# Kernel tuning notes

Measured on AMD Instinct MI355X. Metric: run time of the kernel, lower is better.

The kernel has to match this reference:

```python
import math
import jax, jax.numpy as jnp
import numpy as np

B, N, C = 4, 2048, 256
KMAX, RATIO, ITERS, H = 1024, 12.0, 3, 4
TAU, SIG_FLOOR, INIT_SIG_MIX, INIT_OFF, JIT = 1.0, 0.03, 0.1, 0.5, 1e-6
W_KL, W_ENT, W_OCC, W_COL = 0.05, 0.0, 0.5, 0.1
K_USE = min(max(1, math.ceil(N / RATIO)), KMAX)  # 171
EPS = 1e-8


def _sym(M):
    return 0.5 * (M + jnp.swapaxes(M, -1, -2))


def _l2n(x):
    return x / jnp.maximum(jnp.linalg.norm(x, axis=-1, keepdims=True), 1e-12)


def _ln(x, g, b):
    m = x.mean(-1, keepdims=True)
    v = ((x - m) ** 2).mean(-1, keepdims=True)
    return (x - m) / jnp.sqrt(v + 1e-5) * g + b


def setup_inputs():
    key = jax.random.key(0)
    ks = jax.random.split(key, 16)
    s = jax.random.normal(ks[0], (B, N, C), jnp.float32)
    mu = jax.random.normal(ks[1], (B, N, 3), jnp.float32)
    # per-point SPD covariances (Sigma must be PSD for the overlap solve)
    L = jax.random.normal(ks[2], (B, N, 3, 3), jnp.float32) * 0.3
    Sigma = L @ jnp.swapaxes(L, -1, -2) + 0.05 * jnp.eye(3, dtype=jnp.float32)
    mask = jnp.ones((B, N), jnp.float32)
    lim = 1.0 / math.sqrt(C)
    u = lambda k, sh: jax.random.uniform(k, sh, jnp.float32, -lim, lim)
    return dict(
        s=s, mu=mu, Sigma=Sigma, mask=mask,
        slot_embed_pool=jax.random.normal(ks[3], (KMAX, C), jnp.float32) * 0.02,
        geo_offsets_pool=jax.random.normal(ks[4], (KMAX, 3), jnp.float32) * 0.5,
        gating_W=u(ks[5], (C, C)), proj_q_W=u(ks[6], (C, C)), proj_k_W=u(ks[7], (C, C)),
        gru_w_ih=u(ks[8], (3 * C, C)), gru_w_hh=u(ks[9], (3 * C, C)),
        gru_b_ih=u(ks[10], (3 * C,)), gru_b_hh=u(ks[11], (3 * C,)),
        ln_g=jnp.ones((C,), jnp.float32), ln_b=jnp.zeros((C,), jnp.float32),
        mlp_w1=u(ks[12], (4 * C, C)), mlp_b1=u(ks[13], (4 * C,)),
        mlp_w2=u(ks[14], (C, 4 * C)), mlp_b2=u(ks[15], (C,)),
        w_geo=jnp.float32(1.0),
        geo_scale_raw=jnp.full((H,), -4.0, jnp.float32),
        geo_bias=jnp.full((H,), -6.0, jnp.float32),
    )


def _forward(s, mu, Sigma, mask, slot_embed_pool, geo_offsets_pool, gating_W,
             proj_q_W, proj_k_W, gru_w_ih, gru_w_hh, gru_b_ih, gru_b_hh,
             ln_g, ln_b, mlp_w1, mlp_b1, mlp_w2, mlp_b2,
             w_geo, geo_scale_raw, geo_bias):
    I3 = jnp.eye(3, dtype=s.dtype)
    m1 = mask[:, :, None]                    # [B,N,1]
    cnt = jnp.maximum(mask.sum(1), EPS)      # [B]

    # ---- slot selection (eval mode: no gate noise, rand_slots=0) ----
    s_global = (s * m1).sum(1) / cnt[:, None]
    q = _l2n(s_global @ gating_W.T)
    kn = _l2n(slot_embed_pool)
    scores = q @ kn.T                        # [B,KMAX]
    idx = jax.lax.top_k(scores, K_USE)[1]    # [B,K]
    slots = slot_embed_pool[idx]             # [B,K,C]
    geo_off = geo_offsets_pool[idx]          # [B,K,3]

    # ---- masked mean/std of mu ----
    mean = (mu * m1).sum(1) / cnt[:, None]   # [B,3]
    dm = mu - mean[:, None, :]
    cov = jnp.einsum('bni,bnj->bij', dm * m1, dm) / cnt[:, None, None]
    cov = _sym(cov)
    std = jnp.sqrt(jnp.maximum(jnp.diagonal(cov, axis1=-2, axis2=-1), EPS))
    std = jnp.maximum(std, SIG_FLOOR)
    mu_k = mean[:, None, :] + geo_off * (INIT_OFF * std[:, None, :])

    Sig_avg = _sym((Sigma * m1[..., None]).sum(1) / cnt[:, None, None])
    Sig_k = jnp.broadcast_to(Sig_avg[:, None] * INIT_SIG_MIX, (B, K_USE, 3, 3))
    Sig_k = Sig_k + (SIG_FLOOR ** 2) * I3 + JIT * I3

    k_sem = s @ proj_k_W.T                   # [B,N,C]
    a_h = jax.nn.softplus(geo_scale_raw)     # [H]
    A = None
    for _ in range(ITERS):
        q_sem = slots @ proj_q_W.T           # [B,K,C]
        logits_sem = jnp.einsum('bnc,bkc->bnk', k_sem, q_sem) / math.sqrt(C)
        delta = mu[:, :, None, :] - mu_k[:, None, :, :]       # [B,N,K,3]
        sig_sum = Sigma[:, :, None] + Sig_k[:, None]          # [B,N,K,3,3]
        sol = jnp.linalg.solve(sig_sum, delta[..., None])[..., 0]
        maha = (delta * sol).sum(-1)
        logdet = jnp.linalg.slogdet(sig_sum)[1]
        G = -0.5 * (maha + logdet)                            # [B,N,K]
        geo = (a_h[None, :, None, None] * G[:, None] + geo_bias[None, :, None, None]).sum(1)
        logits = (logits_sem + w_geo * geo) / max(TAU, 1e-6)
        logits = jnp.where(m1 < 0.5, -1e9, logits)
        A = jax.nn.softmax(logits, axis=-1) * m1              # [B,N,K]
        # moment-matching merge (A already mask-weighted; matches torch A*mask)
        occ = jnp.maximum(A.sum(1), EPS)                      # [B,K]
        mu_k = jnp.einsum('bnk,bni->bki', A, mu) / occ[..., None]
        d = mu[:, :, None, :] - mu_k[:, None, :, :]
        outer = d[..., :, None] * d[..., None, :]             # [B,N,K,3,3]
        Sig_k = (jnp.einsum('bnk,bnij->bkij', A, Sigma)
                 + jnp.einsum('bnk,bnkij->bkij', A, outer)) / occ[:, :, None, None]
        Sig_k = _sym(Sig_k) + max(JIT, 1e-6) * I3
        dg = jnp.diagonal(Sig_k, axis1=-2, axis2=-1)
        dg_f = jnp.maximum(dg, SIG_FLOOR ** 2)
        Sig_k = Sig_k - I3 * dg[..., None, :] + I3 * dg_f[..., None, :]
        Sig_k = _sym(Sig_k) + JIT * I3
        denom = jnp.maximum(A.sum(1), 1e-8)
        slot_in = jnp.einsum('bnk,bnc->bkc', A, s) / denom[..., None]
        # GRU cell
        x = slot_in.reshape(-1, C)
        h = slots.reshape(-1, C)
        gi = x @ gru_w_ih.T + gru_b_ih
        gh = h @ gru_w_hh.T + gru_b_hh
        r = jax.nn.sigmoid(gi[:, :C] + gh[:, :C])
        z = jax.nn.sigmoid(gi[:, C:2 * C] + gh[:, C:2 * C])
        n = jnp.tanh(gi[:, 2 * C:] + r * gh[:, 2 * C:])
        slots = ((1.0 - z) * n + z * h).reshape(B, K_USE, C)
        xm = _ln(slots, ln_g, ln_b)
        slots = slots + (jax.nn.gelu(xm @ mlp_w1.T + mlp_b1, approximate=False) @ mlp_w2.T + mlp_b2)

    # ---- losses ----
    hist = jnp.zeros((KMAX,), jnp.float32).at[idx.reshape(-1)].add(1.0)
    p = hist / jnp.maximum(hist.sum(), 1.0)
    pc = jnp.maximum(p, 1e-8)
    usage_kl = (pc * (jnp.log(pc) - math.log(1.0 / KMAX))).sum()
    usage_neg_ent = (pc * jnp.log(pc)).sum()
    occ2 = (A * m1).sum(1)
    occ2 = occ2 / jnp.maximum(occ2.sum(-1, keepdims=True), 1e-8)
    occ_mse = ((occ2 - 1.0 / K_USE) ** 2).mean()
    X = jnp.swapaxes(A * m1, 1, 2)           # [B,K,N]
    Xn = X / jnp.maximum(jnp.linalg.norm(X, axis=-1, keepdims=True), 1e-8)
    Gm = jnp.einsum('bkn,bln->bkl', Xn, Xn)
    eyeK = jnp.eye(K_USE, dtype=A.dtype)[None]
    off = (Gm - eyeK) * (1.0 - eyeK)
    col = (off ** 2).mean()
    total = W_KL * usage_kl + W_ENT * usage_neg_ent + W_OCC * occ_mse + W_COL * col
    return (A, slots, mu_k, Sig_k, idx, usage_kl, usage_neg_ent, occ_mse, col, total)


def reference(s, mu, Sigma, mask, slot_embed_pool, geo_offsets_pool, gating_W,
              proj_q_W, proj_k_W, gru_w_ih, gru_w_hh, gru_b_ih, gru_b_hh,
              ln_g, ln_b, mlp_w1, mlp_b1, mlp_w2, mlp_b2,
              w_geo, geo_scale_raw, geo_bias):
    return _forward(s, mu, Sigma, mask, slot_embed_pool, geo_offsets_pool, gating_W,
                    proj_q_W, proj_k_W, gru_w_ih, gru_w_hh, gru_b_ih, gru_b_hh,
                    ln_g, ln_b, mlp_w1, mlp_b1, mlp_w2, mlp_b2,
                    w_geo, geo_scale_raw, geo_bias)
```

## Files before the change

kernel.cpp:

```cpp
#include <hip/hip_runtime.h>
#include <math.h>

#define B_ 4
#define N_ 2048
#define C_ 256
#define KMAX_ 1024
#define KU_ 171
#define BK_ 684
#define ITERS_ 3
#define H_ 4
#define EPS_ 1e-8f
#define SIGF_ 0.03f
#define JIT_ 1e-6f
#define LOGKMAX_ 6.93147180559945f

#define WS_CNT 0
#define WS_MUS 4
#define WS_MOS 16
#define WS_SGS 40
#define WS_COLACC 100
#define WS_SSUM 128
#define WS_STATS_BYTES (1152*4)
#define WS_MEAN 1152
#define WS_STD 1164
#define WS_SIGAVG 1176
#define WS_IDXI 1216
#define WS_KSEM 1920
#define WS_QSEM (WS_KSEM+2097152)
#define WS_OCC  (WS_QSEM+175104)
#define WS_PART (WS_OCC+704)
#define WS_W2P  WS_PART
#define WS_GBUF (WS_PART+1400832)
#define WS_ATA  WS_GBUF
#define WS_SNEW (WS_GBUF+700416)
#define WS_HID  (WS_SNEW+175104)
#define WS_ACPART (WS_HID+700416)
#define WS_QV   (WS_ACPART+28160)
#define WS_SCORE (WS_QV+1024)

#define O_A 0
#define O_SLOTS 1400832
#define O_MUK   1575936
#define O_SIGK  1577988
#define O_IDX   1584144
#define O_KL    1584828
#define O_ENT   1584829
#define O_OCC   1584830
#define O_COL   1584831
#define O_TOT   1584832

__device__ __forceinline__ float wred(float v) {
  #pragma unroll
  for (int i = 32; i; i >>= 1) v += __shfl_xor(v, i);
  return v;
}
__device__ __forceinline__ float wmax(float v) {
  #pragma unroll
  for (int i = 32; i; i >>= 1) v = fmaxf(v, __shfl_xor(v, i));
  return v;
}

__device__ __forceinline__ float blk_red(float v, float* red, int t) {
  red[t] = v; __syncthreads();
  #pragma unroll
  for (int s = 128; s > 0; s >>= 1) {
    if (t < s) red[t] += red[t + s];
    __syncthreads();
  }
  float r = red[0]; __syncthreads();
  return r;
}

__global__ __launch_bounds__(256) void k_mom(const float* __restrict__ mu,
    const float* __restrict__ Sigma, const float* __restrict__ mask,
    float* __restrict__ ws) {
  int blk = blockIdx.x; int b = blk / 8; int nc = blk % 8; int t = threadIdx.x;
  int n = nc * 256 + t;
  float m = mask[b * N_ + n];
  const float* mun = mu + ((size_t)(b * N_ + n)) * 3;
  float m0 = mun[0], m1v = mun[1], m2 = mun[2];
  const float* sgn = Sigma + ((size_t)(b * N_ + n)) * 9;
  float sg[9];
  #pragma unroll
  for (int j = 0; j < 9; j++) sg[j] = sgn[j];
  int lane = t & 63;
  float vals[19];
  vals[0] = m; vals[1] = m * m0; vals[2] = m * m1v; vals[3] = m * m2;
  vals[4] = m * m0 * m0; vals[5] = m * m0 * m1v; vals[6] = m * m0 * m2;
  vals[7] = m * m1v * m1v; vals[8] = m * m1v * m2; vals[9] = m * m2 * m2;
  #pragma unroll
  for (int j = 0; j < 9; j++) vals[10 + j] = m * sg[j];
  #pragma unroll
  for (int j = 0; j < 19; j++) {
    float v = wred(vals[j]);
    if (lane == 0) {
      int base = (j == 0) ? WS_CNT + b : (j < 4 ? WS_MUS + b * 3 + (j - 1)
                 : (j < 10 ? WS_MOS + b * 6 + (j - 4) : WS_SGS + b * 9 + (j - 10)));
      atomicAdd(ws + base, v);
    }
  }
}

__global__ __launch_bounds__(256) void k_ssum(const float* __restrict__ s,
    const float* __restrict__ mask, float* __restrict__ ws) {
  int blk = blockIdx.x; int b = blk / 64; int nc = blk % 64; int t = threadIdx.x;
  const float* sb = s + ((size_t)b * N_ + nc * 32) * C_;
  const float* mk = mask + b * N_ + nc * 32;
  float sa = 0.f;
  #pragma unroll 8
  for (int nn = 0; nn < 32; nn++) sa += mk[nn] * sb[(size_t)nn * C_ + t];
  atomicAdd(ws + WS_SSUM + b * C_ + t, sa);
}

__global__ __launch_bounds__(256) void k_qv(float* __restrict__ ws,
    const float* __restrict__ gW, float* __restrict__ qv_o) {
  int b = blockIdx.x, t = threadIdx.x;
  __shared__ float sb[C_];
  __shared__ float rv[256];
  sb[t] = ws[WS_SSUM + b * C_ + t];
  __syncthreads();
  if (blockIdx.x == 0 && t < B_) {
    int bb = t;
    float cnt = fmaxf(ws[WS_CNT + bb], EPS_);
    float me[3];
    #pragma unroll
    for (int i = 0; i < 3; i++) { me[i] = ws[WS_MUS + bb * 3 + i] / cnt; ws[WS_MEAN + bb * 3 + i] = me[i]; }
    const int dg[3] = {0, 3, 5};
    #pragma unroll
    for (int i = 0; i < 3; i++) {
      float cov = ws[WS_MOS + bb * 6 + dg[i]] / cnt - me[i] * me[i];
      ws[WS_STD + bb * 3 + i] = fmaxf(sqrtf(fmaxf(cov, EPS_)), SIGF_);
    }
    #pragma unroll
    for (int i = 0; i < 3; i++)
      #pragma unroll
      for (int j = 0; j < 3; j++)
        ws[WS_SIGAVG + bb * 9 + i * 3 + j] =
            0.5f * (ws[WS_SGS + bb * 9 + i * 3 + j] + ws[WS_SGS + bb * 9 + j * 3 + i]) / cnt;
  }
  const float4* g4 = (const float4*)(gW + (size_t)t * C_);
  float qr = 0.f;
  #pragma unroll 4
  for (int c4 = 0; c4 < 64; c4++) {
    float4 g = g4[c4];
    qr += sb[c4 * 4] * g.x + sb[c4 * 4 + 1] * g.y + sb[c4 * 4 + 2] * g.z + sb[c4 * 4 + 3] * g.w;
  }
  float n2 = blk_red(qr * qr, rv, t);
  qv_o[b * C_ + t] = qr / fmaxf(sqrtf(n2), 1e-12f);
}

__global__ __launch_bounds__(256) void k_score(const float* __restrict__ qv,
    const float* __restrict__ pool, float* __restrict__ score) {
  int blk = blockIdx.x; int b = blk >> 4; int pc = blk & 15;
  int t = threadIdx.x; int row = pc * 64 + (t >> 2); int q = t & 3;
  __shared__ float qs[C_];
  qs[t] = qv[b * C_ + t];
  __syncthreads();
  const float4* p4 = (const float4*)(pool + (size_t)row * C_ + q * 64);
  float d = 0.f, p2 = 0.f;
  #pragma unroll
  for (int i = 0; i < 16; i++) {
    float4 pv = p4[i];
    int c = q * 64 + i * 4;
    d += qs[c] * pv.x + qs[c + 1] * pv.y + qs[c + 2] * pv.z + qs[c + 3] * pv.w;
    p2 += pv.x * pv.x + pv.y * pv.y + pv.z * pv.z + pv.w * pv.w;
  }
  d += __shfl_xor(d, 1); d += __shfl_xor(d, 2);
  p2 += __shfl_xor(p2, 1); p2 += __shfl_xor(p2, 2);
  if (q == 0) score[b * KMAX_ + row] = d / fmaxf(sqrtf(p2), 1e-12f);
}

__global__ __launch_bounds__(256) void k_sort(const float* __restrict__ score,
    int* __restrict__ idx_o, float* __restrict__ idxf_o) {
  int b = blockIdx.x, t = threadIdx.x;
  __shared__ float val[KMAX_]; __shared__ int id[KMAX_];
  for (int j = t; j < KMAX_; j += 256) { val[j] = score[b * KMAX_ + j]; id[j] = j; }
  __syncthreads();
  for (int kk = 2; kk <= KMAX_; kk <<= 1) {
    for (int j = kk >> 1; j > 0; j >>= 1) {
      for (int i = t; i < KMAX_; i += 256) {
        int ix = i ^ j;
        if (ix > i) {
          float va = val[i], vb = val[ix]; int ia = id[i], ib = id[ix];
          bool bBeforeA = (vb > va) || (vb == va && ib < ia);
          bool up = ((i & kk) == 0);
          if (up == bBeforeA) {
            val[i] = vb; val[ix] = va; id[i] = ib; id[ix] = ia;
          }
        }
      }
      __syncthreads();
    }
  }
  if (t < KU_) {
    idx_o[b * KU_ + t] = id[t];
    idxf_o[b * KU_ + t] = (float)id[t];
  }
}

__global__ __launch_bounds__(256) void k_init(const int* __restrict__ idx,
    const float* __restrict__ pool, const float* __restrict__ geop,
    const float* __restrict__ ws, float* __restrict__ slots,
    float* __restrict__ mu_k, float* __restrict__ sig_k) {
  int blk = blockIdx.x; int b = blk / KU_, k = blk % KU_; int t = threadIdx.x;
  int j = idx[b * KU_ + k];
  slots[((size_t)(b * KU_ + k)) * C_ + t] = pool[(size_t)j * C_ + t];
  if (t < 3) {
    mu_k[(b * KU_ + k) * 3 + t] = ws[WS_MEAN + b * 3 + t] + geop[j * 3 + t] * (0.5f * ws[WS_STD + b * 3 + t]);
  }
  if (t < 9) {
    float v = ws[WS_SIGAVG + b * 9 + t] * 0.1f;
    if (t == 0 || t == 4 || t == 8) v += SIGF_ * SIGF_ + JIT_;
    sig_k[((size_t)(b * KU_ + k)) * 9 + t] = v;
  }
}

__global__ __launch_bounds__(256) void k_gemm32(const float* __restrict__ in,
    const float* __restrict__ W, float* __restrict__ out, int R) {
  __shared__ float sm[32 * C_];
  int t = threadIdx.x; int r0 = blockIdx.x * 32;
  for (int i = t; i < 32 * 64; i += 256) {
    int rr = i >> 6; int r = r0 + rr;
    float4 v = {0.f, 0.f, 0.f, 0.f};
    if (r < R) v = ((const float4*)(in + (size_t)r * C_))[i & 63];
    ((float4*)sm)[i] = v;
  }
  __syncthreads();
  int cg = t & 63, rg = t >> 6;
  const float4* w0 = (const float4*)(W + (size_t)cg * C_);
  const float4* w1 = (const float4*)(W + (size_t)(cg + 64) * C_);
  const float4* w2 = (const float4*)(W + (size_t)(cg + 128) * C_);
  const float4* w3 = (const float4*)(W + (size_t)(cg + 192) * C_);
  const float4* sm4 = (const float4*)sm;
  float acc[8][4];
  #pragma unroll
  for (int a = 0; a < 8; a++)
    #pragma unroll
    for (int j = 0; j < 4; j++) acc[a][j] = 0.f;
  for (int c4 = 0; c4 < 64; c4++) {
    float4 a0 = w0[c4], a1 = w1[c4], a2 = w2[c4], a3 = w3[c4];
    #pragma unroll
    for (int a = 0; a < 8; a++) {
      float4 sv = sm4[(rg * 8 + a) * 64 + c4];
      acc[a][0] += sv.x * a0.x + sv.y * a0.y + sv.z * a0.z + sv.w * a0.w;
      acc[a][1] += sv.x * a1.x + sv.y * a1.y + sv.z * a1.z + sv.w * a1.w;
      acc[a][2] += sv.x * a2.x + sv.y * a2.y + sv.z * a2.z + sv.w * a2.w;
      acc[a][3] += sv.x * a3.x + sv.y * a3.y + sv.z * a3.z + sv.w * a3.w;
    }
  }
  #pragma unroll
  for (int a = 0; a < 8; a++) {
    int r = r0 + rg * 8 + a;
    if (r < R) {
      out[(size_t)r * C_ + cg]       = acc[a][0];
      out[(size_t)r * C_ + cg + 64]  = acc[a][1];
      out[(size_t)r * C_ + cg + 128] = acc[a][2];
      out[(size_t)r * C_ + cg + 192] = acc[a][3];
    }
  }
}

#define LG32 32
__global__ __launch_bounds__(256) void k_lgsm(const float* __restrict__ ksem,
    const float* __restrict__ qsem, const float* __restrict__ mu,
    const float* __restrict__ Sigma, const float* __restrict__ mask,
    const float* __restrict__ mu_k, const float* __restrict__ sig_k,
    const float* __restrict__ wgeo, const float* __restrict__ gsr,
    const float* __restrict__ gbias, float* __restrict__ A) {
  __shared__ float ksm[LG32 * C_];
  __shared__ float Asm[LG32][176];
  __shared__ float muk[KU_ * 3];
  __shared__ float sgk[KU_ * 6];
  __shared__ float rowd[LG32][10];
  int blk = blockIdx.x; int b = blk / (N_ / LG32); int nt = blk % (N_ / LG32);
  int t = threadIdx.x; int r0 = nt * LG32;
  for (int i = t; i < LG32 * 64; i += 256) {
    int rr = i >> 6;
    ((float4*)ksm)[i] = ((const float4*)(ksem + ((size_t)(b * N_ + r0 + rr)) * C_))[i & 63];
  }
  for (int i = t; i < KU_ * 3; i += 256) muk[i] = mu_k[(size_t)b * KU_ * 3 + i];
  for (int i = t; i < KU_ * 6; i += 256) {
    int k = i / 6, c = i % 6;
    const int map[6] = {0, 1, 2, 4, 5, 8};
    sgk[i] = sig_k[((size_t)(b * KU_ + k)) * 9 + map[c]];
  }
  for (int i = t; i < LG32 * 10; i += 256) {
    int rr = i / 10, c = i % 10;
    int n = r0 + rr;
    float v;
    if (c == 0) v = mask[b * N_ + n];
    else if (c < 4) v = mu[((size_t)(b * N_ + n)) * 3 + (c - 1)];
    else {
      const int map[6] = {0, 1, 2, 4, 5, 8};
      v = Sigma[((size_t)(b * N_ + n)) * 9 + map[c - 4]];
    }
    rowd[rr][c] = v;
  }
  __syncthreads();
  int kg = t & 63, rg = t >> 6;
  int k0i = kg, k1i = kg + 64, k2i = kg + 128;
  bool v2 = (k2i < KU_);
  const float* qbase = qsem + (size_t)b * KU_ * C_;
  const float4* q0 = (const float4*)(qbase + (size_t)k0i * C_);
  const float4* q1 = (const float4*)(qbase + (size_t)k1i * C_);
  const float4* q2 = (const float4*)(qbase + (size_t)(v2 ? k2i : k0i) * C_);
  const float4* sm4 = (const float4*)ksm;
  float acc[8][3];
  #pragma unroll
  for (int a = 0; a < 8; a++) { acc[a][0] = 0.f; acc[a][1] = 0.f; acc[a][2] = 0.f; }
  for (int c4 = 0; c4 < 64; c4++) {
    float4 qa = q0[c4], qb = q1[c4], qc = q2[c4];
    #pragma unroll
    for (int a = 0; a < 8; a++) {
      float4 sv = sm4[(rg * 8 + a) * 64 + c4];
      acc[a][0] += sv.x * qa.x + sv.y * qa.y + sv.z * qa.z + sv.w * qa.w;
      acc[a][1] += sv.x * qb.x + sv.y * qb.y + sv.z * qb.z + sv.w * qb.w;
      acc[a][2] += sv.x * qc.x + sv.y * qc.y + sv.z * qc.z + sv.w * qc.w;
    }
  }
  float ah = 0.f, bs = 0.f;
  #pragma unroll
  for (int h = 0; h < H_; h++) {
    float x = gsr[h];
    ah += fmaxf(x, 0.f) + log1pf(expf(-fabsf(x)));
    bs += gbias[h];
  }
  float wg = wgeo[0];
  #pragma unroll
  for (int kk = 0; kk < 3; kk++) {
    int k = kg + kk * 64;
    if (kk == 2 && !v2) break;
    float mk0 = muk[k * 3], mk1 = muk[k * 3 + 1], mk2 = muk[k * 3 + 2];
    float s0 = sgk[k * 6], s1 = sgk[k * 6 + 1], s2 = sgk[k * 6 + 2];
    float s3 = sgk[k * 6 + 3], s4 = sgk[k * 6 + 4], s5 = sgk[k * 6 + 5];
    #pragma unroll
    for (int a = 0; a < 8; a++) {
      int row = rg * 8 + a;
      float m = rowd[row][0];
      float d0 = rowd[row][1] - mk0, d1 = rowd[row][2] - mk1, d2 = rowd[row][3] - mk2;
      float s00 = rowd[row][4] + s0, s01 = rowd[row][5] + s1, s02 = rowd[row][6] + s2;
      float s11 = rowd[row][7] + s3, s12 = rowd[row][8] + s4, s22 = rowd[row][9] + s5;
      float c00 = s11 * s22 - s12 * s12;
      float c01 = s02 * s12 - s01 * s22;
      float c02 = s01 * s12 - s02 * s11;
      float det = s00 * c00 + s01 * c01 + s02 * c02;
      float c11 = s00 * s22 - s02 * s02;
      float c12 = s01 * s02 - s00 * s12;
      float c22 = s00 * s11 - s01 * s01;
      float inv = 1.0f / det;
      float x0 = (c00 * d0 + c01 * d1 + c02 * d2) * inv;
      float x1 = (c01 * d0 + c11 * d1 + c12 * d2) * inv;
      float x2 = (c02 * d0 + c12 * d1 + c22 * d2) * inv;
      float maha = d0 * x0 + d1 * x1 + d2 * x2;
      float logdet = logf(fmaxf(det, 1e-30f));
      float G = -0.5f * (maha + logdet);
      float l = acc[a][kk] * 0.0625f + wg * (ah * G + bs);
      if (m < 0.5f) l = -1e9f;
      Asm[row][k] = l;
    }
  }
  __syncthreads();
  int w = t >> 6, lane = t & 63;
  #pragma unroll
  for (int q = 0; q < 8; q++) {
    int a = w * 8 + q;
    float v0 = (lane < KU_) ? Asm[a][lane] : -INFINITY;
    float v1 = (lane + 64 < KU_) ? Asm[a][lane + 64] : -INFINITY;
    float vv2 = (lane + 128 < KU_) ? Asm[a][lane + 128] : -INFINITY;
    float mx = wmax(fmaxf(v0, fmaxf(v1, vv2)));
    float e0 = (lane < KU_) ? expf(v0 - mx) : 0.f;
    float e1 = (lane + 64 < KU_) ? expf(v1 - mx) : 0.f;
    float e2 = (lane + 128 < KU_) ? expf(vv2 - mx) : 0.f;
    float ss = wred(e0 + e1 + e2);
    float scale = rowd[a][0] / ss;
    if (lane < KU_) Asm[a][lane] = e0 * scale;
    if (lane + 64 < KU_) Asm[a][lane + 64] = e1 * scale;
    if (lane + 128 < KU_) Asm[a][lane + 128] = e2 * scale;
  }
  __syncthreads();
  for (int i = t; i < LG32 * KU_; i += 256) {
    int a = i / KU_, k = i - a * KU_;
    A[((size_t)(b * N_ + r0 + a)) * KU_ + k] = Asm[a][k];
  }
}

#define AC_NC 4
__global__ __launch_bounds__(256) void k_amoms(const float* __restrict__ A,
    const float* __restrict__ mu, const float* __restrict__ Sigma,
    const float* __restrict__ s, float* __restrict__ acpart,
    float* __restrict__ atpart) {
  __shared__ float shm[1024];
  __shared__ float red2[4][16][10];
  int t = threadIdx.x;
  if (blockIdx.x < 176) {
    int blk = blockIdx.x;
    int nc = blk & 3; int tmp = blk >> 2; int kt = tmp % 11; int b = tmp / 11;
    int nn = t >> 4; int kk = t & 15;
    int k = kt * 16 + kk;
    float S[10];
    #pragma unroll
    for (int i = 0; i < 10; i++) S[i] = 0.f;
    float (*rowd)[10] = (float(*)[10])shm;
    const int NCH = N_ / AC_NC;
    for (int n0 = nc * NCH; n0 < nc * NCH + NCH; n0 += 16) {
      __syncthreads();
      if (t < 144) {
        int rr = t / 9, c = t % 9;
        int n = n0 + rr;
        float v;
        if (c < 3) v = mu[((size_t)(b * N_ + n)) * 3 + c];
        else {
          const int map[6] = {0, 1, 2, 4, 5, 8};
          v = Sigma[((size_t)(b * N_ + n)) * 9 + map[c - 3]];
        }
        rowd[rr][c] = v;
      }
      float a = (k < KU_) ? A[((size_t)(b * N_ + n0 + nn)) * KU_ + k] : 0.f;
      __syncthreads();
      float m0 = rowd[nn][0], m1 = rowd[nn][1], m2 = rowd[nn][2];
      float g0 = rowd[nn][3], g1 = rowd[nn][4], g2 = rowd[nn][5];
      float g4 = rowd[nn][6], g5 = rowd[nn][7], g8 = rowd[nn][8];
      S[0] += a; S[1] += a * m0; S[2] += a * m1; S[3] += a * m2;
      S[4] += a * (g0 + m0 * m0); S[5] += a * (g1 + m0 * m1); S[6] += a * (g2 + m0 * m2);
      S[7] += a * (g4 + m1 * m1); S[8] += a * (g5 + m1 * m2); S[9] += a * (g8 + m2 * m2);
    }
    #pragma unroll
    for (int i = 0; i < 10; i++) { S[i] += __shfl_xor(S[i], 16); S[i] += __shfl_xor(S[i], 32); }
    int w = t >> 6, lane = t & 63;
    if (lane < 16) {
      #pragma unroll
      for (int i = 0; i < 10; i++) red2[w][lane][i] = S[i];
    }
    __syncthreads();
    if (t < 160) {
      int k2 = t / 10, i = t % 10;
      float v = red2[0][k2][i] + red2[1][k2][i] + red2[2][k2][i] + red2[3][k2][i];
      acpart[(((size_t)nc * B_ + b) * 176 + kt * 16 + k2) * 10 + i] = v;
    }
  } else {
    int blk = blockIdx.x - 176;
    int nc = blk & 7; int tmp = blk >> 3; int kt = tmp % 11; int b = tmp / 11;
    int k0 = kt * 16;
    float* Ach = shm;
    float acc[16];
    #pragma unroll
    for (int j = 0; j < 16; j++) acc[j] = 0.f;
    for (int n0 = nc * 256; n0 < nc * 256 + 256; n0 += 64) {
      __syncthreads();
      for (int i = t; i < 64 * 16; i += 256) {
        int nn = i >> 4, kk = i & 15; int k = k0 + kk;
        Ach[i] = (k < KU_) ? A[((size_t)(b * N_ + n0 + nn)) * KU_ + k] : 0.f;
      }
      __syncthreads();
      for (int nn = 0; nn < 64; nn++) {
        float xv = s[((size_t)(b * N_ + n0 + nn)) * C_ + t];
        #pragma unroll
        for (int j = 0; j < 16; j++) acc[j] += Ach[(nn << 4) + j] * xv;
      }
    }
    #pragma unroll
    for (int j = 0; j < 16; j++) {
      int k = k0 + j;
      if (k < KU_) atpart[((size_t)nc * (B_ * KU_) + b * KU_ + k) * C_ + t] = acc[j];
    }
  }
}

__global__ __launch_bounds__(256) void k_gg(const float* __restrict__ atpart,
    const float* __restrict__ acpart, const float* __restrict__ slots,
    const float* __restrict__ wih, const float* __restrict__ bih,
    const float* __restrict__ whh, const float* __restrict__ bhh,
    float* __restrict__ gbuf, float* __restrict__ occ,
    float* __restrict__ mu_k, float* __restrict__ sig_k) {
  int t = threadIdx.x;
  if (blockIdx.x >= 86) {
    if (blockIdx.y != 0) return;
    int i = (blockIdx.x - 86) * 256 + t;
    if (i >= B_ * KU_) return;
    int b = i / KU_, k = i % KU_;
    float p[10];
    #pragma unroll
    for (int j = 0; j < 10; j++) {
      float v = 0.f;
      #pragma unroll
      for (int nc = 0; nc < AC_NC; nc++)
        v += acpart[(((size_t)nc * B_ + b) * 176 + k) * 10 + j];
      p[j] = v;
    }
    float o = p[0];
    occ[b * KU_ + k] = o;
    float oc = fmaxf(o, EPS_);
    float s1x = p[1], s1y = p[2], s1z = p[3];
    float q0 = s1x / oc, q1 = s1y / oc, q2 = s1z / oc;
    mu_k[(b * KU_ + k) * 3 + 0] = q0;
    mu_k[(b * KU_ + k) * 3 + 1] = q1;
    mu_k[(b * KU_ + k) * 3 + 2] = q2;
    float v00 = (p[4] - 2.f * q0 * s1x + o * q0 * q0) / oc + JIT_;
    float v01 = (p[5] - q0 * s1y - s1x * q1 + o * q0 * q1) / oc;
    float v02 = (p[6] - q0 * s1z - s1x * q2 + o * q0 * q2) / oc;
    float v11 = (p[7] - 2.f * q1 * s1y + o * q1 * q1) / oc + JIT_;
    float v12 = (p[8] - q1 * s1z - s1y * q2 + o * q1 * q2) / oc;
    float v22 = (p[9] - 2.f * q2 * s1z + o * q2 * q2) / oc + JIT_;
    v00 = fmaxf(v00, SIGF_ * SIGF_) + JIT_;
    v11 = fmaxf(v11, SIGF_ * SIGF_) + JIT_;
    v22 = fmaxf(v22, SIGF_ * SIGF_) + JIT_;
    float* po = sig_k + ((size_t)(b * KU_ + k)) * 9;
    po[0] = v00; po[1] = v01; po[2] = v02;
    po[3] = v01; po[4] = v11; po[5] = v12;
    po[6] = v02; po[7] = v12; po[8] = v22;
    return;
  }
  int p = blockIdx.y; int r0 = blockIdx.x * 8;
  __shared__ float sx[8 * C_];
  __shared__ float sh[8 * C_];
  __shared__ float socc[8];
  bool needx = (p < 3), needh = (p != 2);
  if (t < 8) {
    int r = r0 + t;
    float o = 0.f;
    if (r < BK_) {
      int b = r / KU_, k = r % KU_;
      #pragma unroll
      for (int nc = 0; nc < AC_NC; nc++)
        o += acpart[(((size_t)nc * B_ + b) * 176 + k) * 10];
    }
    socc[t] = fmaxf(o, 1e-8f);
  }
  __syncthreads();
  for (int i = t; i < 8 * C_; i += 256) {
    int rr = i >> 8, c = i & 255;
    int r = r0 + rr;
    if (r < BK_) {
      if (needx) {
        float v = 0.f;
        #pragma unroll
        for (int nc = 0; nc < 8; nc++) v += atpart[((size_t)nc * BK_ + r) * C_ + c];
        sx[i] = v / socc[rr];
      }
      if (needh) sh[i] = slots[(size_t)r * C_ + c];
    } else {
      if (needx) sx[i] = 0.f;
      if (needh) sh[i] = 0.f;
    }
  }
  __syncthreads();
  int grow = (p >= 2) ? 512 + t : p * 256 + t;
  float acc[8];
  #pragma unroll
  for (int a = 0; a < 8; a++) acc[a] = 0.f;
  const float4* sx4 = (const float4*)sx;
  const float4* sh4 = (const float4*)sh;
  if (p < 2) {
    const float4* wi = (const float4*)(wih + (size_t)grow * C_);
    const float4* wh = (const float4*)(whh + (size_t)grow * C_);
    for (int c4 = 0; c4 < 64; c4++) {
      float4 a1 = wi[c4], a2 = wh[c4];
      #pragma unroll
      for (int a = 0; a < 8; a++) {
        float4 xv = sx4[a * 64 + c4], hv = sh4[a * 64 + c4];
        acc[a] += xv.x * a1.x + xv.y * a1.y + xv.z * a1.z + xv.w * a1.w
                + hv.x * a2.x + hv.y * a2.y + hv.z * a2.z + hv.w * a2.w;
      }
    }
  } else if (p == 2) {
    const float4* wi = (const float4*)(wih + (size_t)grow * C_);
    for (int c4 = 0; c4 < 64; c4++) {
      float4 a1 = wi[c4];
      #pragma unroll
      for (int a = 0; a < 8; a++) {
        float4 xv = sx4[a * 64 + c4];
        acc[a] += xv.x * a1.x + xv.y * a1.y + xv.z * a1.z + xv.w * a1.w;
      }
    }
  } else {
    const float4* wh = (const float4*)(whh + (size_t)grow * C_);
    for (int c4 = 0; c4 < 64; c4++) {
      float4 a2 = wh[c4];
      #pragma unroll
      for (int a = 0; a < 8; a++) {
        float4 hv = sh4[a * 64 + c4];
        acc[a] += hv.x * a2.x + hv.y * a2.y + hv.z * a2.z + hv.w * a2.w;
      }
    }
  }
  float bias = (p < 2) ? (bih[grow] + bhh[grow]) : ((p == 2) ? bih[grow] : bhh[grow]);
  #pragma unroll
  for (int a = 0; a < 8; a++) {
    int r = r0 + a;
    if (r < BK_) gbuf[((size_t)p * BK_ + r) * C_ + t] = acc[a] + bias;
  }
}

__global__ __launch_bounds__(256) void k_w1ln(const float* __restrict__ gbuf,
    const float* __restrict__ slots, const float* __restrict__ lng,
    const float* __restrict__ lnb, const float* __restrict__ w1p,
    const float* __restrict__ b1p, float* __restrict__ snew,
    float* __restrict__ hid) {
  int r0 = blockIdx.x * 4; int t = threadIdx.x; int oc = blockIdx.y * 256 + t;
  __shared__ float ssn[4 * C_];
  __shared__ float sxm[4 * C_];
  bool wr = (blockIdx.y == 0);
  for (int i = t; i < 4 * C_; i += 256) {
    int rr = i >> 8, c = i & 255;
    int r = r0 + rr;
    float gr = gbuf[((size_t)0 * BK_ + r) * C_ + c];
    float gz = gbuf[((size_t)1 * BK_ + r) * C_ + c];
    float gi = gbuf[((size_t)2 * BK_ + r) * C_ + c];
    float gh = gbuf[((size_t)3 * BK_ + r) * C_ + c];
    float rg = 1.f / (1.f + expf(-gr));
    float z = 1.f / (1.f + expf(-gz));
    float n = tanhf(gi + rg * gh);
    float h = slots[(size_t)r * C_ + c];
    float sn = (1.f - z) * n + z * h;
    ssn[i] = sn;
    if (wr) snew[(size_t)r * C_ + c] = sn;
  }
  __syncthreads();
  {
    int w = t >> 6, lane = t & 63;
    float x0 = ssn[w * 256 + lane], x1 = ssn[w * 256 + lane + 64];
    float x2 = ssn[w * 256 + lane + 128], x3 = ssn[w * 256 + lane + 192];
    float mean = wred(x0 + x1 + x2 + x3) * (1.f / 256.f);
    float d0 = x0 - mean, d1 = x1 - mean, d2 = x2 - mean, d3 = x3 - mean;
    float var = wred(d0 * d0 + d1 * d1 + d2 * d2 + d3 * d3) * (1.f / 256.f);
    float rstd = rsqrtf(var + 1e-5f);
    sxm[w * 256 + lane]       = d0 * rstd * lng[lane]       + lnb[lane];
    sxm[w * 256 + lane + 64]  = d1 * rstd * lng[lane + 64]  + lnb[lane + 64];
    sxm[w * 256 + lane + 128] = d2 * rstd * lng[lane + 128] + lnb[lane + 128];
    sxm[w * 256 + lane + 192] = d3 * rstd * lng[lane + 192] + lnb[lane + 192];
  }
  __syncthreads();
  const float4* W4 = (const float4*)(w1p + (size_t)oc * C_);
  const float4* sm4 = (const float4*)sxm;
  float acc[4] = {0, 0, 0, 0};
  for (int c4 = 0; c4 < 64; c4++) {
    float4 wv = W4[c4];
    #pragma unroll
    for (int a = 0; a < 4; a++) {
      float4 sv = sm4[a * 64 + c4];
      acc[a] += sv.x * wv.x + sv.y * wv.y + sv.z * wv.z + sv.w * wv.w;
    }
  }
  float bb = b1p[oc];
  #pragma unroll
  for (int a = 0; a < 4; a++) {
    float v = acc[a] + bb;
    hid[(size_t)(r0 + a) * 1024 + oc] = 0.5f * v * (1.f + erff(v * 0.70710678118654752f));
  }
}

__global__ __launch_bounds__(256) void k_w2p(const float* __restrict__ hid,
    const float* __restrict__ w2p, float* __restrict__ w2part) {
  int r0 = blockIdx.x * 4; int kc = blockIdx.y; int t = threadIdx.x;
  __shared__ float sm[4 * C_];
  for (int i = t; i < 4 * 64; i += 256) {
    int rr = i >> 6;
    ((float4*)sm)[i] = ((const float4*)(hid + (size_t)(r0 + rr) * 1024 + kc * 256))[i & 63];
  }
  __syncthreads();
  const float4* W4 = (const float4*)(w2p + (size_t)t * 1024 + kc * 256);
  const float4* sm4 = (const float4*)sm;
  float acc[4] = {0, 0, 0, 0};
  for (int c4 = 0; c4 < 64; c4++) {
    float4 wv = W4[c4];
    #pragma unroll
    for (int a = 0; a < 4; a++) {
      float4 sv = sm4[a * 64 + c4];
      acc[a] += sv.x * wv.x + sv.y * wv.y + sv.z * wv.z + sv.w * wv.w;
    }
  }
  #pragma unroll
  for (int a = 0; a < 4; a++)
    w2part[((size_t)kc * BK_ + r0 + a) * C_ + t] = acc[a];
}

__global__ __launch_bounds__(256) void k_qsemf(const float* __restrict__ snew,
    const float* __restrict__ w2part, const float* __restrict__ b2p,
    const float* __restrict__ qWp, float* __restrict__ slots,
    float* __restrict__ qsem) {
  int r0 = blockIdx.x * 4; int t = threadIdx.x;
  __shared__ float sfin[4 * C_];
  for (int i = t; i < 4 * C_; i += 256) {
    int rr = i >> 8, c = i & 255;
    int r = r0 + rr;
    float v = snew[(size_t)r * C_ + c] + b2p[c];
    #pragma unroll
    for (int kc = 0; kc < 4; kc++) v += w2part[((size_t)kc * BK_ + r) * C_ + c];
    sfin[i] = v;
    slots[(size_t)r * C_ + c] = v;
  }
  __syncthreads();
  const float4* qr = (const float4*)(qWp + (size_t)t * C_);
  const float4* s4 = (const float4*)sfin;
  float o[4] = {0, 0, 0, 0};
  for (int c4 = 0; c4 < 64; c4++) {
    float4 wv = qr[c4];
    #pragma unroll
    for (int a = 0; a < 4; a++) {
      float4 xv = s4[a * 64 + c4];
      o[a] += xv.x * wv.x + xv.y * wv.y + xv.z * wv.z + xv.w * wv.w;
    }
  }
  #pragma unroll
  for (int a = 0; a < 4; a++)
    qsem[(size_t)(r0 + a) * C_ + t] = o[a];
}

__global__ __launch_bounds__(256) void k_atn(const float* __restrict__ A,
    const float* __restrict__ X, float* __restrict__ out, int NX) {
  int blk = blockIdx.x;
  int nc = blk & 7; int tmp = blk >> 3; int kt = tmp % 11; int b = tmp / 11;
  int t = threadIdx.x; int k0 = kt * 16;
  __shared__ float Ach[64 * 16];
  float acc[16];
  #pragma unroll
  for (int j = 0; j < 16; j++) acc[j] = 0.f;
  for (int n0 = nc * 256; n0 < nc * 256 + 256; n0 += 64) {
    __syncthreads();
    for (int i = t; i < 64 * 16; i += 256) {
      int nn = i >> 4, kk = i & 15; int k = k0 + kk;
      Ach[i] = (k < KU_) ? A[((size_t)(b * N_ + n0 + nn)) * KU_ + k] : 0.f;
    }
    __syncthreads();
    if (t < NX) {
      for (int nn = 0; nn < 64; nn++) {
        float xv = X[((size_t)(b * N_ + n0 + nn)) * NX + t];
        #pragma unroll
        for (int j = 0; j < 16; j++) acc[j] += Ach[(nn << 4) + j] * xv;
      }
    }
  }
  if (t < NX) {
    #pragma unroll
    for (int j = 0; j < 16; j++) {
      int k = k0 + j;
      if (k < KU_) atomicAdd(&out[((size_t)(b * KU_ + k)) * NX + t], acc[j]);
    }
  }
}

__global__ __launch_bounds__(256) void k_histocc(const int* __restrict__ idx,
    const float* __restrict__ occ, float* __restrict__ okl,
    float* __restrict__ oent, float* __restrict__ oocc) {
  int t = threadIdx.x;
  __shared__ float buf[KMAX_];
  __shared__ float red[256];
  if (blockIdx.x == 0) {
    for (int i = t; i < KMAX_; i += 256) buf[i] = 0.f;
    __syncthreads();
    for (int i = t; i < B_ * KU_; i += 256) atomicAdd(&buf[idx[i]], 1.0f);
    __syncthreads();
    float kl = 0.f, ent = 0.f;
    const float tot = (float)(B_ * KU_);
    for (int i = t; i < KMAX_; i += 256) {
      float pc = fmaxf(buf[i] / tot, 1e-8f);
      float lp = logf(pc);
      kl += pc * (lp + LOGKMAX_);
      ent += pc * lp;
    }
    kl = blk_red(kl, red, t); ent = blk_red(ent, red, t);
    if (t == 0) { okl[0] = kl; oent[0] = ent; }
  } else {
    for (int i = t; i < B_ * KU_; i += 256) buf[i] = occ[i];
    __syncthreads();
    __shared__ float bsum[B_];
    for (int b = 0; b < B_; b++) {
      float s = 0.f;
      for (int i = t; i < KU_; i += 256) s += buf[b * KU_ + i];
      s = blk_red(s, red, t);
      if (t == 0) bsum[b] = fmaxf(s, 1e-8f);
      __syncthreads();
    }
    float acc = 0.f;
    const float invK = 1.0f / (float)KU_;
    for (int i = t; i < B_ * KU_; i += 256) {
      int b = i / KU_;
      float v = buf[i] / bsum[b] - invK;
      acc += v * v;
    }
    acc = blk_red(acc, red, t);
    if (t == 0) oocc[0] = acc / (float)(B_ * KU_);
  }
}

__global__ __launch_bounds__(256) void k_colpart(const float* __restrict__ AtA,
    float* __restrict__ colacc) {
  int blk = blockIdx.x; int b = blk / KU_, k = blk % KU_; int t = threadIdx.x;
  float acc = 0.f;
  if (t < KU_ && t != k) {
    float dk = AtA[((size_t)(b * KU_ + k)) * KU_ + k];
    float dt = AtA[((size_t)(b * KU_ + t)) * KU_ + t];
    float v  = AtA[((size_t)(b * KU_ + k)) * KU_ + t];
    float gm = v / (fmaxf(sqrtf(dk), 1e-8f) * fmaxf(sqrtf(dt), 1e-8f));
    acc = gm * gm;
  }
  float v = wred(acc);
  __shared__ float p[4];
  if ((t & 63) == 0) p[t >> 6] = v;
  __syncthreads();
  if (t == 0) atomicAdd(colacc, p[0] + p[1] + p[2] + p[3]);
}

__global__ void k_colfin(const float* __restrict__ colacc,
    const float* __restrict__ okl, const float* __restrict__ oent,
    const float* __restrict__ oocc, float* __restrict__ ocol, float* __restrict__ otot) {
  float col = colacc[0] / (float)(B_ * KU_ * KU_);
  ocol[0] = col;
  otot[0] = 0.05f * okl[0] + 0.0f * oent[0] + 0.5f * oocc[0] + 0.1f * col;
}

extern "C" void kernel_launch(void* const* d_in, const int* in_sizes, int n_in,
                              void* d_out_v, int out_size, void* d_ws, size_t ws_size,
                              hipStream_t stream) {
  const float* s     = (const float*)d_in[0];
  const float* mu    = (const float*)d_in[1];
  const float* Sigma = (const float*)d_in[2];
  const float* mask  = (const float*)d_in[3];
  const float* pool  = (const float*)d_in[4];
  const float* geop  = (const float*)d_in[5];
  const float* gW    = (const float*)d_in[6];
  const float* qW    = (const float*)d_in[7];
  const float* kW    = (const float*)d_in[8];
  const float* wih   = (const float*)d_in[9];
  const float* whh   = (const float*)d_in[10];
  const float* bih   = (const float*)d_in[11];
  const float* bhh   = (const float*)d_in[12];
  const float* lng   = (const float*)d_in[13];
  const float* lnb   = (const float*)d_in[14];
  const float* w1    = (const float*)d_in[15];
  const float* b1    = (const float*)d_in[16];
  const float* w2    = (const float*)d_in[17];
  const float* b2    = (const float*)d_in[18];
  const float* wgeo  = (const float*)d_in[19];
  const float* gsr   = (const float*)d_in[20];
  const float* gbias = (const float*)d_in[21];

  float* out = (float*)d_out_v;
  float* A     = out + O_A;
  float* slots = out + O_SLOTS;
  float* muk   = out + O_MUK;
  float* sigk  = out + O_SIGK;
  float* idxf  = out + O_IDX;
  float* okl   = out + O_KL;
  float* oent  = out + O_ENT;
  float* oocc  = out + O_OCC;
  float* ocol  = out + O_COL;
  float* otot  = out + O_TOT;

  float* ws = (float*)d_ws;
  int*   idxi   = (int*)(ws + WS_IDXI);
  float* ksem   = ws + WS_KSEM;
  float* qsem   = ws + WS_QSEM;
  float* occ    = ws + WS_OCC;
  float* atpart = ws + WS_PART;
  float* gbuf   = ws + WS_GBUF;
  float* snew   = ws + WS_SNEW;
  float* hid    = ws + WS_HID;
  float* w2part = ws + WS_W2P;
  float* acpart = ws + WS_ACPART;
  float* ata    = ws + WS_ATA;
  float* colacc = ws + WS_COLACC;

  hipMemsetAsync(ws, 0, WS_STATS_BYTES, stream);
  k_mom<<<B_ * 8, 256, 0, stream>>>(mu, Sigma, mask, ws);
  k_ssum<<<B_ * 64, 256, 0, stream>>>(s, mask, ws);
  k_qv<<<B_, 256, 0, stream>>>(ws, gW, ws + WS_QV);
  k_score<<<B_ * 16, 256, 0, stream>>>(ws + WS_QV, pool, ws + WS_SCORE);
  k_sort<<<B_, 256, 0, stream>>>(ws + WS_SCORE, idxi, idxf);
  k_init<<<B_ * KU_, 256, 0, stream>>>(idxi, pool, geop, ws, slots, muk, sigk);

  k_gemm32<<<(B_ * N_) / 32, 256, 0, stream>>>(s, kW, ksem, B_ * N_);
  k_gemm32<<<(BK_ + 31) / 32, 256, 0, stream>>>(slots, qW, qsem, BK_);

  for (int it = 0; it < ITERS_; ++it) {
    k_lgsm<<<B_ * (N_ / LG32), 256, 0, stream>>>(ksem, qsem, mu, Sigma, mask,
                                                 muk, sigk, wgeo, gsr, gbias, A);
    k_amoms<<<176 + 352, 256, 0, stream>>>(A, mu, Sigma, s, acpart, atpart);
    k_gg<<<dim3(89, 4), 256, 0, stream>>>(atpart, acpart, slots, wih, bih, whh, bhh,
                                          gbuf, occ, muk, sigk);
    k_w1ln<<<dim3(171, 4), 256, 0, stream>>>(gbuf, slots, lng, lnb, w1, b1, snew, hid);
    k_w2p<<<dim3(171, 4), 256, 0, stream>>>(hid, w2, w2part);
    k_qsemf<<<171, 256, 0, stream>>>(snew, w2part, b2, qW, slots, qsem);
  }

  hipMemsetAsync(ata, 0, (size_t)B_ * KU_ * KU_ * 4, stream);
  k_atn<<<B_ * 11 * 8, 256, 0, stream>>>(A, A, ata, KU_);
  k_colpart<<<B_ * KU_, 256, 0, stream>>>(ata, colacc);
  k_histocc<<<2, 256, 0, stream>>>(idxi, occ, okl, oent, oocc);
  k_colfin<<<1, 1, 0, stream>>>(colacc, okl, oent, oocc, ocol, otot);
}
```

Before: 811.2 us.

## Retile logits GEMM with staged transposed query chunks and smaller row tiles

The logits kernel now uses 16-row tiles (double the blocks) and stages 32-channel chunks of both keys and queries in shared memory. Queries are stored transposed, so each thread computes a 4x4 register tile of consecutive slots, where before each thread read three query rows directly from global memory. The GRU gate kernel is also remapped so each thread computes two output columns for four rows instead of one column for eight rows. The aim is better data reuse and fewer uncoalesced global loads, at the cost of more barriers per chunk and scalar transposed stores into shared memory.

```diff
diff --git a/kernel.cpp b/kernel.cpp
--- a/kernel.cpp
+++ b/kernel.cpp
@@ -260,32 +260,28 @@
   }
 }
 
-#define LG32 32
 __global__ __launch_bounds__(256) void k_lgsm(const float* __restrict__ ksem,
     const float* __restrict__ qsem, const float* __restrict__ mu,
     const float* __restrict__ Sigma, const float* __restrict__ mask,
     const float* __restrict__ mu_k, const float* __restrict__ sig_k,
     const float* __restrict__ wgeo, const float* __restrict__ gsr,
     const float* __restrict__ gbias, float* __restrict__ A) {
-  __shared__ float ksm[LG32 * C_];
-  __shared__ float Asm[LG32][176];
+  __shared__ float qchT[32][172];
+  __shared__ float ksm[16][36];
+  __shared__ float Asm[16][176];
   __shared__ float muk[KU_ * 3];
   __shared__ float sgk[KU_ * 6];
-  __shared__ float rowd[LG32][10];
-  int blk = blockIdx.x; int b = blk / (N_ / LG32); int nt = blk % (N_ / LG32);
-  int t = threadIdx.x; int r0 = nt * LG32;
-  for (int i = t; i < LG32 * 64; i += 256) {
-    int rr = i >> 6;
-    ((float4*)ksm)[i] = ((const float4*)(ksem + ((size_t)(b * N_ + r0 + rr)) * C_))[i & 63];
-  }
+  __shared__ float rowd[16][10];
+  int blk = blockIdx.x; int b = blk / (N_ / 16); int nt = blk % (N_ / 16);
+  int t = threadIdx.x; int r0 = nt * 16;
   for (int i = t; i < KU_ * 3; i += 256) muk[i] = mu_k[(size_t)b * KU_ * 3 + i];
   for (int i = t; i < KU_ * 6; i += 256) {
     int k = i / 6, c = i % 6;
     const int map[6] = {0, 1, 2, 4, 5, 8};
     sgk[i] = sig_k[((size_t)(b * KU_ + k)) * 9 + map[c]];
   }
-  for (int i = t; i < LG32 * 10; i += 256) {
-    int rr = i / 10, c = i % 10;
+  if (t < 160) {
+    int rr = t / 10, c = t % 10;
     int n = r0 + rr;
     float v;
     if (c == 0) v = mask[b * N_ + n];
@@ -296,26 +292,45 @@
     }
     rowd[rr][c] = v;
   }
-  __syncthreads();
   int kg = t & 63, rg = t >> 6;
-  int k0i = kg, k1i = kg + 64, k2i = kg + 128;
-  bool v2 = (k2i < KU_);
-  const float* qbase = qsem + (size_t)b * KU_ * C_;
-  const float4* q0 = (const float4*)(qbase + (size_t)k0i * C_);
-  const float4* q1 = (const float4*)(qbase + (size_t)k1i * C_);
-  const float4* q2 = (const float4*)(qbase + (size_t)(v2 ? k2i : k0i) * C_);
-  const float4* sm4 = (const float4*)ksm;
-  float acc[8][3];
-  #pragma unroll
-  for (int a = 0; a < 8; a++) { acc[a][0] = 0.f; acc[a][1] = 0.f; acc[a][2] = 0.f; }
-  for (int c4 = 0; c4 < 64; c4++) {
-    float4 qa = q0[c4], qb = q1[c4], qc = q2[c4];
-    #pragma unroll
-    for (int a = 0; a < 8; a++) {
-      float4 sv = sm4[(rg * 8 + a) * 64 + c4];
-      acc[a][0] += sv.x * qa.x + sv.y * qa.y + sv.z * qa.z + sv.w * qa.w;
-      acc[a][1] += sv.x * qb.x + sv.y * qb.y + sv.z * qb.z + sv.w * qb.w;
-      acc[a][2] += sv.x * qc.x + sv.y * qc.y + sv.z * qc.z + sv.w * qc.w;
+  float acc[4][4];
+  #pragma unroll
+  for (int a = 0; a < 4; a++)
+    #pragma unroll
+    for (int j = 0; j < 4; j++) acc[a][j] = 0.f;
+  const float4* qT4 = (const float4*)&qchT[0][0];
+  const float4* km4 = (const float4*)&ksm[0][0];
+  for (int cc = 0; cc < 8; cc++) {
+    __syncthreads();
+    for (int i = t; i < 16 * 8; i += 256) {
+      int rr = i >> 3, c4 = i & 7;
+      float4 v = ((const float4*)(ksem + ((size_t)(b * N_ + r0 + rr)) * C_ + cc * 32))[c4];
+      ((float4*)&ksm[rr][0])[0];
+      ksm[rr][c4 * 4 + 0] = v.x; ksm[rr][c4 * 4 + 1] = v.y;
+      ksm[rr][c4 * 4 + 2] = v.z; ksm[rr][c4 * 4 + 3] = v.w;
+    }
+    for (int i = t; i < 172 * 8; i += 256) {
+      int k = i >> 3, c4 = i & 7;
+      float4 v = {0.f, 0.f, 0.f, 0.f};
+      if (k < KU_) v = ((const float4*)(qsem + ((size_t)(b * KU_ + k)) * C_ + cc * 32))[c4];
+      qchT[c4 * 4 + 0][k] = v.x; qchT[c4 * 4 + 1][k] = v.y;
+      qchT[c4 * 4 + 2][k] = v.z; qchT[c4 * 4 + 3][k] = v.w;
+    }
+    __syncthreads();
+    #pragma unroll
+    for (int c4 = 0; c4 < 8; c4++) {
+      float4 q0 = qT4[(c4 * 4 + 0) * 43 + kg];
+      float4 q1 = qT4[(c4 * 4 + 1) * 43 + kg];
+      float4 q2 = qT4[(c4 * 4 + 2) * 43 + kg];
+      float4 q3 = qT4[(c4 * 4 + 3) * 43 + kg];
+      #pragma unroll
+      for (int a = 0; a < 4; a++) {
+        float4 av = km4[(rg * 4 + a) * 9 + c4];
+        acc[a][0] += av.x * q0.x + av.y * q1.x + av.z * q2.x + av.w * q3.x;
+        acc[a][1] += av.x * q0.y + av.y * q1.y + av.z * q2.y + av.w * q3.y;
+        acc[a][2] += av.x * q0.z + av.y * q1.z + av.z * q2.z + av.w * q3.z;
+        acc[a][3] += av.x * q0.w + av.y * q1.w + av.z * q2.w + av.w * q3.w;
+      }
     }
   }
   float ah = 0.f, bs = 0.f;
@@ -326,51 +341,54 @@
     bs += gbias[h];
   }
   float wg = wgeo[0];
-  #pragma unroll
-  for (int kk = 0; kk < 3; kk++) {
-    int k = kg + kk * 64;
-    if (kk == 2 && !v2) break;
-    float mk0 = muk[k * 3], mk1 = muk[k * 3 + 1], mk2 = muk[k * 3 + 2];
-    float s0 = sgk[k * 6], s1 = sgk[k * 6 + 1], s2 = sgk[k * 6 + 2];
-    float s3 = sgk[k * 6 + 3], s4 = sgk[k * 6 + 4], s5 = sgk[k * 6 + 5];
-    #pragma unroll
-    for (int a = 0; a < 8; a++) {
-      int row = rg * 8 + a;
-      float m = rowd[row][0];
-      float d0 = rowd[row][1] - mk0, d1 = rowd[row][2] - mk1, d2 = rowd[row][3] - mk2;
-      float s00 = rowd[row][4] + s0, s01 = rowd[row][5] + s1, s02 = rowd[row][6] + s2;
-      float s11 = rowd[row][7] + s3, s12 = rowd[row][8] + s4, s22 = rowd[row][9] + s5;
-      float c00 = s11 * s22 - s12 * s12;
-      float c01 = s02 * s12 - s01 * s22;
-      float c02 = s01 * s12 - s02 * s11;
-      float det = s00 * c00 + s01 * c01 + s02 * c02;
-      float c11 = s00 * s22 - s02 * s02;
-      float c12 = s01 * s02 - s00 * s12;
-      float c22 = s00 * s11 - s01 * s01;
-      float inv = 1.0f / det;
-      float x0 = (c00 * d0 + c01 * d1 + c02 * d2) * inv;
-      float x1 = (c01 * d0 + c11 * d1 + c12 * d2) * inv;
-      float x2 = (c02 * d0 + c12 * d1 + c22 * d2) * inv;
-      float maha = d0 * x0 + d1 * x1 + d2 * x2;
-      float logdet = logf(fmaxf(det, 1e-30f));
-      float G = -0.5f * (maha + logdet);
-      float l = acc[a][kk] * 0.0625f + wg * (ah * G + bs);
-      if (m < 0.5f) l = -1e9f;
-      Asm[row][k] = l;
+  if (kg < 43) {
+    #pragma unroll
+    for (int kk = 0; kk < 4; kk++) {
+      int k = kg * 4 + kk;
+      if (k < KU_) {
+        float mk0 = muk[k * 3], mk1 = muk[k * 3 + 1], mk2 = muk[k * 3 + 2];
+        float s0 = sgk[k * 6], s1 = sgk[k * 6 + 1], s2 = sgk[k * 6 + 2];
+        float s3 = sgk[k * 6 + 3], s4 = sgk[k * 6 + 4], s5 = sgk[k * 6 + 5];
+        #pragma unroll
+        for (int a = 0; a < 4; a++) {
+          int row = rg * 4 + a;
+          float m = rowd[row][0];
+          float d0 = rowd[row][1] - mk0, d1 = rowd[row][2] - mk1, d2 = rowd[row][3] - mk2;
+          float s00 = rowd[row][4] + s0, s01 = rowd[row][5] + s1, s02 = rowd[row][6] + s2;
+          float s11 = rowd[row][7] + s3, s12 = rowd[row][8] + s4, s22 = rowd[row][9] + s5;
+          float c00 = s11 * s22 - s12 * s12;
+          float c01 = s02 * s12 - s01 * s22;
+          float c02 = s01 * s12 - s02 * s11;
+          float det = s00 * c00 + s01 * c01 + s02 * c02;
+          float c11 = s00 * s22 - s02 * s02;
+          float c12 = s01 * s02 - s00 * s12;
+          float c22 = s00 * s11 - s01 * s01;
+          float inv = 1.0f / det;
+          float x0 = (c00 * d0 + c01 * d1 + c02 * d2) * inv;
+          float x1 = (c01 * d0 + c11 * d1 + c12 * d2) * inv;
+          float x2 = (c02 * d0 + c12 * d1 + c22 * d2) * inv;
+          float maha = d0 * x0 + d1 * x1 + d2 * x2;
+          float logdet = logf(fmaxf(det, 1e-30f));
+          float G = -0.5f * (maha + logdet);
+          float l = acc[a][kk] * 0.0625f + wg * (ah * G + bs);
+          if (m < 0.5f) l = -1e9f;
+          Asm[row][k] = l;
+        }
+      }
     }
   }
   __syncthreads();
   int w = t >> 6, lane = t & 63;
   #pragma unroll
-  for (int q = 0; q < 8; q++) {
-    int a = w * 8 + q;
+  for (int q = 0; q < 4; q++) {
+    int a = w * 4 + q;
     float v0 = (lane < KU_) ? Asm[a][lane] : -INFINITY;
     float v1 = (lane + 64 < KU_) ? Asm[a][lane + 64] : -INFINITY;
-    float vv2 = (lane + 128 < KU_) ? Asm[a][lane + 128] : -INFINITY;
-    float mx = wmax(fmaxf(v0, fmaxf(v1, vv2)));
+    float v2 = (lane + 128 < KU_) ? Asm[a][lane + 128] : -INFINITY;
+    float mx = wmax(fmaxf(v0, fmaxf(v1, v2)));
     float e0 = (lane < KU_) ? expf(v0 - mx) : 0.f;
     float e1 = (lane + 64 < KU_) ? expf(v1 - mx) : 0.f;
-    float e2 = (lane + 128 < KU_) ? expf(vv2 - mx) : 0.f;
+    float e2 = (lane + 128 < KU_) ? expf(v2 - mx) : 0.f;
     float ss = wred(e0 + e1 + e2);
     float scale = rowd[a][0] / ss;
     if (lane < KU_) Asm[a][lane] = e0 * scale;
@@ -378,7 +396,7 @@
     if (lane + 128 < KU_) Asm[a][lane + 128] = e2 * scale;
   }
   __syncthreads();
-  for (int i = t; i < LG32 * KU_; i += 256) {
+  for (int i = t; i < 16 * KU_; i += 256) {
     int a = i / KU_, k = i - a * KU_;
     A[((size_t)(b * N_ + r0 + a)) * KU_ + k] = Asm[a][k];
   }
@@ -544,50 +562,65 @@
     }
   }
   __syncthreads();
-  int grow = (p >= 2) ? 512 + t : p * 256 + t;
-  float acc[8];
-  #pragma unroll
-  for (int a = 0; a < 8; a++) acc[a] = 0.f;
+  int cg = t & 127, rg2 = t >> 7;
+  int base = (p >= 2) ? 512 : p * 256;
+  int col0 = base + cg, col1 = base + cg + 128;
+  float acc0[4] = {0, 0, 0, 0}, acc1[4] = {0, 0, 0, 0};
   const float4* sx4 = (const float4*)sx;
   const float4* sh4 = (const float4*)sh;
   if (p < 2) {
-    const float4* wi = (const float4*)(wih + (size_t)grow * C_);
-    const float4* wh = (const float4*)(whh + (size_t)grow * C_);
+    const float4* wi0 = (const float4*)(wih + (size_t)col0 * C_);
+    const float4* wi1 = (const float4*)(wih + (size_t)col1 * C_);
+    const float4* wh0 = (const float4*)(whh + (size_t)col0 * C_);
+    const float4* wh1 = (const float4*)(whh + (size_t)col1 * C_);
     for (int c4 = 0; c4 < 64; c4++) {
-      float4 a1 = wi[c4], a2 = wh[c4];
+      float4 a0 = wi0[c4], a1 = wi1[c4], h0 = wh0[c4], h1 = wh1[c4];
       #pragma unroll
-      for (int a = 0; a < 8; a++) {
-        float4 xv = sx4[a * 64 + c4], hv = sh4[a * 64 + c4];
-        acc[a] += xv.x * a1.x + xv.y * a1.y + xv.z * a1.z + xv.w * a1.w
-                + hv.x * a2.x + hv.y * a2.y + hv.z * a2.z + hv.w * a2.w;
+      for (int a = 0; a < 4; a++) {
+        float4 xv = sx4[(rg2 * 4 + a) * 64 + c4], hv = sh4[(rg2 * 4 + a) * 64 + c4];
+        acc0[a] += xv.x * a0.x + xv.y * a0.y + xv.z * a0.z + xv.w * a0.w
+                 + hv.x * h0.x + hv.y * h0.y + hv.z * h0.z + hv.w * h0.w;
+        acc1[a] += xv.x * a1.x + xv.y * a1.y + xv.z * a1.z + xv.w * a1.w
+                 + hv.x * h1.x + hv.y * h1.y + hv.z * h1.z + hv.w * h1.w;
       }
     }
   } else if (p == 2) {
-    const float4* wi = (const float4*)(wih + (size_t)grow * C_);
+    const float4* wi0 = (const float4*)(wih + (size_t)col0 * C_);
+    const float4* wi1 = (const float4*)(wih + (size_t)col1 * C_);
     for (int c4 = 0; c4 < 64; c4++) {
-      float4 a1 = wi[c4];
+      float4 a0 = wi0[c4], a1 = wi1[c4];
       #pragma unroll
-      for (int a = 0; a < 8; a++) {
-        float4 xv = sx4[a * 64 + c4];
-        acc[a] += xv.x * a1.x + xv.y * a1.y + xv.z * a1.z + xv.w * a1.w;
+      for (int a = 0; a < 4; a++) {
+        float4 xv = sx4[(rg2 * 4 + a) * 64 + c4];
+        acc0[a] += xv.x * a0.x + xv.y * a0.y + xv.z * a0.z + xv.w * a0.w;
+        acc1[a] += xv.x * a1.x + xv.y * a1.y + xv.z * a1.z + xv.w * a1.w;
       }
     }
   } else {
-    const float4* wh = (const float4*)(whh + (size_t)grow * C_);
+    const float4* wh0 = (const float4*)(whh + (size_t)col0 * C_);
+    const float4* wh1 = (const float4*)(whh + (size_t)col1 * C_);
     for (int c4 = 0; c4 < 64; c4++) {
-      float4 a2 = wh[c4];
+      float4 h0 = wh0[c4], h1 = wh1[c4];
       #pragma unroll
-      for (int a = 0; a < 8; a++) {
-        float4 hv = sh4[a * 64 + c4];
-        acc[a] += hv.x * a2.x + hv.y * a2.y + hv.z * a2.z + hv.w * a2.w;
-      }
-    }
-  }
-  float bias = (p < 2) ? (bih[grow] + bhh[grow]) : ((p == 2) ? bih[grow] : bhh[grow]);
-  #pragma unroll
-  for (int a = 0; a < 8; a++) {
-    int r = r0 + a;
-    if (r < BK_) gbuf[((size_t)p * BK_ + r) * C_ + t] = acc[a] + bias;
+      for (int a = 0; a < 4; a++) {
+        float4 hv = sh4[(rg2 * 4 + a) * 64 + c4];
+        acc0[a] += hv.x * h0.x + hv.y * h0.y + hv.z * h0.z + hv.w * h0.w;
+        acc1[a] += hv.x * h1.x + hv.y * h1.y + hv.z * h1.z + hv.w * h1.w;
+      }
+    }
+  }
+  float bias0, bias1;
+  if (p < 2) { bias0 = bih[col0] + bhh[col0]; bias1 = bih[col1] + bhh[col1]; }
+  else if (p == 2) { bias0 = bih[col0]; bias1 = bih[col1]; }
+  else { bias0 = bhh[col0]; bias1 = bhh[col1]; }
+  int gc0 = cg, gc1 = cg + 128;
+  #pragma unroll
+  for (int a = 0; a < 4; a++) {
+    int r = r0 + rg2 * 4 + a;
+    if (r < BK_) {
+      gbuf[((size_t)p * BK_ + r) * C_ + gc0] = acc0[a] + bias0;
+      gbuf[((size_t)p * BK_ + r) * C_ + gc1] = acc1[a] + bias1;
+    }
   }
 }
 
@@ -873,8 +906,8 @@
   k_gemm32<<<(BK_ + 31) / 32, 256, 0, stream>>>(slots, qW, qsem, BK_);
 
   for (int it = 0; it < ITERS_; ++it) {
-    k_lgsm<<<B_ * (N_ / LG32), 256, 0, stream>>>(ksem, qsem, mu, Sigma, mask,
-                                                 muk, sigk, wgeo, gsr, gbias, A);
+    k_lgsm<<<B_ * (N_ / 16), 256, 0, stream>>>(ksem, qsem, mu, Sigma, mask,
+                                               muk, sigk, wgeo, gsr, gbias, A);
     k_amoms<<<176 + 352, 256, 0, stream>>>(A, mu, Sigma, s, acpart, atpart);
     k_gg<<<dim3(89, 4), 256, 0, stream>>>(atpart, acpart, slots, wih, bih, whh, bhh,
                                           gbuf, occ, muk, sigk);
```

After: 896.1 us. 1.1x slower.
